# Kernel optimization log

Measured on AMD Instinct MI355X. Metric: run time of the kernel, lower is better.

## Reference

```python
import jax, jax.numpy as jnp
import numpy as np

B, N, DIN, DOUT = 8, 2048, 256, 256
ALPHA = 0.2  # leaky relu slope
EPS = 1e-6


def setup_inputs() -> dict:
    key = jax.random.key(0)
    k1, k2, k3, k4 = jax.random.split(key, 4)
    h = jax.random.normal(k1, (B, N, DIN), dtype=jnp.float32)
    adj = jax.random.uniform(k2, (B, N, N), dtype=jnp.float32)
    # xavier_uniform with gain=1.414
    gain = 1.414
    limW = gain * np.sqrt(6.0 / (DIN + DOUT))
    W = jax.random.uniform(k3, (DIN, DOUT), minval=-limW, maxval=limW, dtype=jnp.float32)
    lima = gain * np.sqrt(6.0 / (2 * DOUT + 1))
    a = jax.random.uniform(k4, (2 * DOUT, 1), minval=-lima, maxval=lima, dtype=jnp.float32)
    return {"h": h, "adj": adj, "W": W, "a": a}


def reference(h, adj, W, a):
    # Wh: [B, N, DOUT]
    Wh = jnp.einsum("bnd,df->bnf", h, W)
    # Split additive attention: cat([Wh_i, Wh_j]) @ a == Wh_i @ a1 + Wh_j @ a2
    a1 = a[:DOUT, 0]   # [DOUT]
    a2 = a[DOUT:, 0]   # [DOUT]
    s1 = Wh @ a1       # [B, N] score contribution of source node i
    s2 = Wh @ a2       # [B, N] score contribution of target node j
    e = s1[:, :, None] + s2[:, None, :]           # [B, N, N]
    e = jnp.where(e > 0, e, ALPHA * e)            # leaky relu
    e = e + jnp.log(adj + EPS)                    # soft adjacency mask
    alpha_w = jax.nn.softmax(e, axis=-1)          # [B, N, N]
    # dropout is identity in eval / deterministic reference
    h_prime = jnp.einsum("bij,bjf->bif", alpha_w, Wh)
    return h_prime
```

## Files before the change

kernel.cpp:

```cpp
#include <hip/hip_runtime.h>
#include <hip/hip_bf16.h>
#include <stdint.h>

#define ALPHA_ 0.2f
#define EPS_   1e-6f

typedef __attribute__((ext_vector_type(8))) short  short8;
typedef __attribute__((ext_vector_type(4))) float  float4v;

static __device__ __forceinline__ unsigned short f2bf(float x) {
    union { float f; unsigned int u; } c; c.f = x;
    return (unsigned short)((c.u + 0x7fffu + ((c.u >> 16) & 1u)) >> 16);
}

__global__ __launch_bounds__(256) void k_wt(const float* __restrict__ W,
                                            unsigned short* __restrict__ WTs) {
    const int g  = blockIdx.x * 256 + threadIdx.x;
    const int fb = g >> 9, kc = (g >> 6) & 7, l = g & 63;
    const int m = l & 15, quad = l >> 4;
    const int f = fb * 16 + m, d0 = kc * 32 + quad * 8;
    unsigned short v[8];
#pragma unroll
    for (int i = 0; i < 8; ++i) v[i] = f2bf(W[(d0 + i) * 256 + f]);
    uint4 o;
    o.x = (unsigned)v[0] | ((unsigned)v[1] << 16);
    o.y = (unsigned)v[2] | ((unsigned)v[3] << 16);
    o.z = (unsigned)v[4] | ((unsigned)v[5] << 16);
    o.w = (unsigned)v[6] | ((unsigned)v[7] << 16);
    *(uint4*)(WTs + (size_t)g * 8) = o;
}

__global__ __launch_bounds__(512) void k_wh(const float* __restrict__ h,
                                            const unsigned short* __restrict__ WTs,
                                            const float* __restrict__ a,
                                            unsigned short* __restrict__ WhS,
                                            float* __restrict__ s1g,
                                            float* __restrict__ s2g) {
    __shared__ __align__(16) unsigned short A_lds[32][264];
    __shared__ __align__(16) unsigned short T_lds[256][40];
    __shared__ float s1p[32], s2p[32];
    const int t    = threadIdx.x;
    const int lane = t & 63;
    const int wv   = t >> 6;
    const int m    = lane & 15;
    const int quad = lane >> 4;
    const int r0   = blockIdx.x * 32;
    const int b    = blockIdx.x >> 6;
    const int jc   = blockIdx.x & 63;
    const int j0   = r0 & 2047;

    if (t < 32) { s1p[t] = 0.f; s2p[t] = 0.f; }

#pragma unroll
    for (int k = 0; k < 4; ++k) {
        const int flat = t + k * 512;
        const int r  = flat >> 6;
        const int d4 = flat & 63;
        float4v hv = *(const float4v*)(h + (size_t)(r0 + r) * 256 + d4 * 4);
        uint2 pk;
        pk.x = (unsigned)f2bf(hv.x) | ((unsigned)f2bf(hv.y) << 16);
        pk.y = (unsigned)f2bf(hv.z) | ((unsigned)f2bf(hv.w) << 16);
        *(uint2*)&A_lds[r][d4 * 4] = pk;
    }
    __syncthreads();

    const int fbase = wv * 32;
    float4v acc[2][2];
#pragma unroll
    for (int it = 0; it < 2; ++it)
#pragma unroll
        for (int ft = 0; ft < 2; ++ft)
#pragma unroll
            for (int r = 0; r < 4; ++r) acc[it][ft][r] = 0.f;

    const unsigned short* wtb = WTs + (size_t)(wv * 2) * 4096 + lane * 8;

#pragma unroll
    for (int kc = 0; kc < 8; ++kc) {
        short8 af0 = *(const short8*)&A_lds[m][kc * 32 + quad * 8];
        short8 af1 = *(const short8*)&A_lds[16 + m][kc * 32 + quad * 8];
#pragma unroll
        for (int ft = 0; ft < 2; ++ft) {
            short8 bf = *(const short8*)(wtb + (size_t)ft * 4096 + kc * 512);
            acc[0][ft] = __builtin_amdgcn_mfma_f32_16x16x32_bf16(af0, bf, acc[0][ft], 0, 0, 0);
            acc[1][ft] = __builtin_amdgcn_mfma_f32_16x16x32_bf16(af1, bf, acc[1][ft], 0, 0, 0);
        }
    }

    float a1v[2], a2v[2];
#pragma unroll
    for (int ft = 0; ft < 2; ++ft) {
        a1v[ft] = a[fbase + ft * 16 + m];
        a2v[ft] = a[256 + fbase + ft * 16 + m];
    }
#pragma unroll
    for (int it = 0; it < 2; ++it) {
#pragma unroll
        for (int reg = 0; reg < 4; ++reg) {
            float v1 = 0.f, v2 = 0.f;
#pragma unroll
            for (int ft = 0; ft < 2; ++ft) {
                const float c = acc[it][ft][reg];
                v1 = fmaf(c, a1v[ft], v1);
                v2 = fmaf(c, a2v[ft], v2);
            }
            v1 += __shfl_xor(v1, 1); v2 += __shfl_xor(v2, 1);
            v1 += __shfl_xor(v1, 2); v2 += __shfl_xor(v2, 2);
            v1 += __shfl_xor(v1, 4); v2 += __shfl_xor(v2, 4);
            v1 += __shfl_xor(v1, 8); v2 += __shfl_xor(v2, 8);
            if (m == 0) {
                const int row = it * 16 + quad * 4 + reg;
                atomicAdd(&s1p[row], v1);
                atomicAdd(&s2p[row], v2);
            }
        }
    }

#pragma unroll
    for (int it = 0; it < 2; ++it)
#pragma unroll
        for (int ft = 0; ft < 2; ++ft)
#pragma unroll
            for (int reg = 0; reg < 4; ++reg)
                T_lds[fbase + ft * 16 + m][it * 16 + quad * 4 + reg] =
                    f2bf(acc[it][ft][reg]);

    __syncthreads();

#pragma unroll
    for (int e = 0; e < 2; ++e) {
        const int idx = e * 512 + t;
        const int fb = idx >> 6, l = idx & 63;
        uint4 v = *(const uint4*)&T_lds[fb * 16 + (l & 15)][(l >> 4) * 8];
        *(uint4*)(WhS + ((size_t)(b * 64 + jc) * 16 + fb) * 512 + l * 8) = v;
    }

    if (t < 32) {
        s1g[(size_t)b * 2048 + j0 + t] = s1p[t];
        s2g[(size_t)b * 2048 + j0 + t] = s2p[t];
    }
}

static __device__ __forceinline__ unsigned pk2bf(float lo, float hi) {
    float2 v; v.x = lo; v.y = hi;
    union { __hip_bfloat162 h2; unsigned u; } cv;
    cv.h2 = __float22bfloat162_rn(v);
    return cv.u;
}

static __device__ __forceinline__ uint2 pquad(float4v av, float4v s2v,
                                              float s1, float& rs) {
    float e0 = s1 + s2v.x, e1 = s1 + s2v.y, e2 = s1 + s2v.z, e3 = s1 + s2v.w;
    e0 = fmaxf(e0, ALPHA_ * e0); e1 = fmaxf(e1, ALPHA_ * e1);
    e2 = fmaxf(e2, ALPHA_ * e2); e3 = fmaxf(e3, ALPHA_ * e3);
    const float p0 = (av.x + EPS_) * __expf(e0);
    const float p1 = (av.y + EPS_) * __expf(e1);
    const float p2 = (av.z + EPS_) * __expf(e2);
    const float p3 = (av.w + EPS_) * __expf(e3);
    rs += (p0 + p1) + (p2 + p3);
    uint2 r;
    r.x = pk2bf(p0, p1);
    r.y = pk2bf(p2, p3);
    return r;
}

__global__ __launch_bounds__(256, 8) void k_attn(const float* __restrict__ adj,
                                                 const unsigned short* __restrict__ WhS,
                                                 const float* __restrict__ s1g,
                                                 const float* __restrict__ s2g,
                                                 float* __restrict__ out) {
    __shared__ __align__(16) unsigned short pbuf[2][16][140];
    __shared__ float rsum_lds[16];

    const int t    = threadIdx.x;
    const int lane = t & 63;
    const int wv   = t >> 6;
    const int m    = lane & 15;
    const int quad = lane >> 4;
    const int blk  = blockIdx.x;
    const int b    = blk & 7;
    const int fh   = (blk >> 3) & 1;
    const int i0   = (blk >> 4) * 16;

    const int ip = t >> 4;
    const int jq = t & 15;

    const float* adjp = adj + (size_t)(b * 2048 + i0 + ip) * 2048 + jq * 8;
    const float* s2p  = s2g + (size_t)b * 2048 + jq * 8;
    const float  s1v  = s1g[(size_t)b * 2048 + i0 + ip];

    const int fbb = fh * 8 + wv * 2;
    const unsigned short* whs = WhS + (size_t)b * 64 * 16 * 512;

    float4v acc[2];
#pragma unroll
    for (int ft = 0; ft < 2; ++ft)
#pragma unroll
        for (int r = 0; r < 4; ++r) acc[ft][r] = 0.f;

    float rs = 0.f;

    float4v adjv[2], s2v[2];
#pragma unroll
    for (int c = 0; c < 2; ++c) {
        adjv[c] = *(const float4v*)(adjp + c * 4);
        s2v[c]  = *(const float4v*)(s2p + c * 4);
    }

    for (int step = 0; step < 16; ++step) {
        const int cur = step & 1;

#pragma unroll
        for (int c = 0; c < 2; ++c) {
            uint2 pk = pquad(adjv[c], s2v[c], s1v, rs);
            *(uint2*)&pbuf[cur][ip][jq * 8 + c * 4] = pk;
        }

        const int ns = (step + 1) & 15;
#pragma unroll
        for (int c = 0; c < 2; ++c) {
            adjv[c] = *(const float4v*)(adjp + (size_t)ns * 128 + c * 4);
            s2v[c]  = *(const float4v*)(s2p + (size_t)ns * 128 + c * 4);
        }

        __syncthreads();

#pragma unroll
        for (int kc = 0; kc < 4; ++kc) {
            const unsigned short* bp =
                whs + ((size_t)((step * 4 + kc) * 16 + fbb)) * 512 + lane * 8;
            short8 bf0 = *(const short8*)bp;
            short8 bf1 = *(const short8*)(bp + 512);
            short8 af  = *(const short8*)&pbuf[cur][m][kc * 32 + quad * 8];
            acc[0] = __builtin_amdgcn_mfma_f32_16x16x32_bf16(af, bf0, acc[0], 0, 0, 0);
            acc[1] = __builtin_amdgcn_mfma_f32_16x16x32_bf16(af, bf1, acc[1], 0, 0, 0);
        }
    }

    rs += __shfl_xor(rs, 1);
    rs += __shfl_xor(rs, 2);
    rs += __shfl_xor(rs, 4);
    rs += __shfl_xor(rs, 8);
    if (jq == 0) rsum_lds[ip] = rs;
    __syncthreads();

#pragma unroll
    for (int reg = 0; reg < 4; ++reg) {
        const int row  = quad * 4 + reg;
        const float iv = 1.0f / rsum_lds[row];
#pragma unroll
        for (int ft = 0; ft < 2; ++ft) {
            const int f = fh * 128 + wv * 32 + ft * 16 + m;
            out[(size_t)(b * 2048 + i0 + row) * 256 + f] = acc[ft][reg] * iv;
        }
    }
}

extern "C" void kernel_launch(void* const* d_in, const int* in_sizes, int n_in,
                              void* d_out, int out_size, void* d_ws, size_t ws_size,
                              hipStream_t stream) {
    const float* h   = (const float*)d_in[0];
    const float* adj = (const float*)d_in[1];
    const float* W   = (const float*)d_in[2];
    const float* a   = (const float*)d_in[3];
    float* out = (float*)d_out;

    unsigned short* WhS = (unsigned short*)d_ws;
    unsigned short* WTs = (unsigned short*)((char*)d_ws + 8388608);
    float*          s1  = (float*)((char*)d_ws + 8388608 + 131072);
    float*          s2  = s1 + 16384;

    k_wt  <<<dim3(32),   dim3(256), 0, stream>>>(W, WTs);
    k_wh  <<<dim3(512),  dim3(512), 0, stream>>>(h, WTs, a, WhS, s1, s2);
    k_attn<<<dim3(2048), dim3(256), 0, stream>>>(adj, WhS, s1, s2, out);
}
```

Before: 267.9 us.

## Build attention probabilities in MFMA operand registers per wave, dropping LDS staging

```diff
diff --git a/kernel.cpp b/kernel.cpp
--- a/kernel.cpp
+++ b/kernel.cpp
@@ -164,94 +164,97 @@
     return r;
 }
 
-__global__ __launch_bounds__(256, 8) void k_attn(const float* __restrict__ adj,
+__global__ __launch_bounds__(256, 4) void k_attn(const float* __restrict__ adj,
                                                  const unsigned short* __restrict__ WhS,
                                                  const float* __restrict__ s1g,
                                                  const float* __restrict__ s2g,
                                                  float* __restrict__ out) {
-    __shared__ __align__(16) unsigned short pbuf[2][16][140];
-    __shared__ float rsum_lds[16];
+    __shared__ __align__(16) float s2_lds[2048];
 
     const int t    = threadIdx.x;
     const int lane = t & 63;
-    const int wv   = t >> 6;
+    const int w    = t >> 6;
     const int m    = lane & 15;
     const int quad = lane >> 4;
     const int blk  = blockIdx.x;
-    const int b    = blk & 7;
-    const int fh   = (blk >> 3) & 1;
-    const int i0   = (blk >> 4) * 16;
-
-    const int ip = t >> 4;
-    const int jq = t & 15;
-
-    const float* adjp = adj + (size_t)(b * 2048 + i0 + ip) * 2048 + jq * 8;
-    const float* s2p  = s2g + (size_t)b * 2048 + jq * 8;
-    const float  s1v  = s1g[(size_t)b * 2048 + i0 + ip];
-
-    const int fbb = fh * 8 + wv * 2;
-    const unsigned short* whs = WhS + (size_t)b * 64 * 16 * 512;
-
-    float4v acc[2];
-#pragma unroll
-    for (int ft = 0; ft < 2; ++ft)
+    const int b     = blk & 7;
+    const int fq    = (blk >> 3) & 3;
+    const int itile = blk >> 5;
+
+    const int irow = itile * 64 + w * 16 + m;
+
+    {
+        const float* s2src = s2g + (size_t)b * 2048;
+        *(float4v*)&s2_lds[t * 8]     = *(const float4v*)(s2src + t * 8);
+        *(float4v*)&s2_lds[t * 8 + 4] = *(const float4v*)(s2src + t * 8 + 4);
+    }
+
+    const float  s1v  = s1g[(size_t)b * 2048 + irow];
+    const float* adjR = adj + (size_t)(b * 2048 + irow) * 2048 + quad * 8;
+    const unsigned short* whs =
+        WhS + (size_t)b * 64 * 16 * 512 + (size_t)(fq * 4) * 512 + lane * 8;
+
+    float4v acc[4];
+#pragma unroll
+    for (int ft = 0; ft < 4; ++ft)
 #pragma unroll
         for (int r = 0; r < 4; ++r) acc[ft][r] = 0.f;
 
     float rs = 0.f;
 
-    float4v adjv[2], s2v[2];
-#pragma unroll
-    for (int c = 0; c < 2; ++c) {
-        adjv[c] = *(const float4v*)(adjp + c * 4);
-        s2v[c]  = *(const float4v*)(s2p + c * 4);
-    }
+    float4v adjv[8];
+#pragma unroll
+    for (int kc = 0; kc < 4; ++kc) {
+        adjv[kc * 2]     = *(const float4v*)(adjR + kc * 32);
+        adjv[kc * 2 + 1] = *(const float4v*)(adjR + kc * 32 + 4);
+    }
+
+    __syncthreads();
 
     for (int step = 0; step < 16; ++step) {
-        const int cur = step & 1;
-
-#pragma unroll
-        for (int c = 0; c < 2; ++c) {
-            uint2 pk = pquad(adjv[c], s2v[c], s1v, rs);
-            *(uint2*)&pbuf[cur][ip][jq * 8 + c * 4] = pk;
+        short8 pa[4];
+#pragma unroll
+        for (int kc = 0; kc < 4; ++kc) {
+            const int jb = step * 128 + kc * 32 + quad * 8;
+            float4v s2a = *(const float4v*)&s2_lds[jb];
+            float4v s2b = *(const float4v*)&s2_lds[jb + 4];
+            uint2 lo = pquad(adjv[kc * 2],     s2a, s1v, rs);
+            uint2 hi = pquad(adjv[kc * 2 + 1], s2b, s1v, rs);
+            union { uint4 u; short8 s; } P;
+            P.u.x = lo.x; P.u.y = lo.y; P.u.z = hi.x; P.u.w = hi.y;
+            pa[kc] = P.s;
         }
 
         const int ns = (step + 1) & 15;
 #pragma unroll
-        for (int c = 0; c < 2; ++c) {
-            adjv[c] = *(const float4v*)(adjp + (size_t)ns * 128 + c * 4);
-            s2v[c]  = *(const float4v*)(s2p + (size_t)ns * 128 + c * 4);
-        }
-
-        __syncthreads();
-
-#pragma unroll
         for (int kc = 0; kc < 4; ++kc) {
-            const unsigned short* bp =
-                whs + ((size_t)((step * 4 + kc) * 16 + fbb)) * 512 + lane * 8;
-            short8 bf0 = *(const short8*)bp;
-            short8 bf1 = *(const short8*)(bp + 512);
-            short8 af  = *(const short8*)&pbuf[cur][m][kc * 32 + quad * 8];
-            acc[0] = __builtin_amdgcn_mfma_f32_16x16x32_bf16(af, bf0, acc[0], 0, 0, 0);
-            acc[1] = __builtin_amdgcn_mfma_f32_16x16x32_bf16(af, bf1, acc[1], 0, 0, 0);
-        }
-    }
-
-    rs += __shfl_xor(rs, 1);
-    rs += __shfl_xor(rs, 2);
-    rs += __shfl_xor(rs, 4);
-    rs += __shfl_xor(rs, 8);
-    if (jq == 0) rsum_lds[ip] = rs;
-    __syncthreads();
+            adjv[kc * 2]     = *(const float4v*)(adjR + (size_t)ns * 128 + kc * 32);
+            adjv[kc * 2 + 1] = *(const float4v*)(adjR + (size_t)ns * 128 + kc * 32 + 4);
+        }
+
+#pragma unroll
+        for (int kc = 0; kc < 4; ++kc) {
+            const unsigned short* bp = whs + (size_t)((step * 4 + kc) * 16) * 512;
+#pragma unroll
+            for (int ft = 0; ft < 4; ++ft) {
+                short8 bf = *(const short8*)(bp + (size_t)ft * 512);
+                acc[ft] = __builtin_amdgcn_mfma_f32_16x16x32_bf16(pa[kc], bf, acc[ft], 0, 0, 0);
+            }
+        }
+    }
+
+    rs += __shfl_xor(rs, 16);
+    rs += __shfl_xor(rs, 32);
 
 #pragma unroll
     for (int reg = 0; reg < 4; ++reg) {
-        const int row  = quad * 4 + reg;
-        const float iv = 1.0f / rsum_lds[row];
-#pragma unroll
-        for (int ft = 0; ft < 2; ++ft) {
-            const int f = fh * 128 + wv * 32 + ft * 16 + m;
-            out[(size_t)(b * 2048 + i0 + row) * 256 + f] = acc[ft][reg] * iv;
+        const float rsum = __shfl(rs, quad * 4 + reg);
+        const float inv  = 1.0f / rsum;
+        const int orow = itile * 64 + w * 16 + quad * 4 + reg;
+#pragma unroll
+        for (int ft = 0; ft < 4; ++ft) {
+            const int f = fq * 64 + ft * 16 + m;
+            out[(size_t)(b * 2048 + orow) * 256 + f] = acc[ft][reg] * inv;
         }
     }
 }
@@ -272,5 +275,5 @@
 
     k_wt  <<<dim3(32),   dim3(256), 0, stream>>>(W, WTs);
     k_wh  <<<dim3(512),  dim3(512), 0, stream>>>(h, WTs, a, WhS, s1, s2);
-    k_attn<<<dim3(2048), dim3(256), 0, stream>>>(adj, WhS, s1, s2, out);
-}
+    k_attn<<<dim3(1024), dim3(256), 0, stream>>>(adj, WhS, s1, s2, out);
+}
```

New measurement: 288.2 us. 7.6% more time.
